# Kernel tuning notes

Measured on AMD Instinct MI355X. Metric: run time of the kernel, lower is better.

The kernel has to match this reference:

```python
import jax, jax.numpy as jnp
import numpy as np

N_POINTS = 2_000_000
IN_CH = 10
UNITS = 32  # out_channels // 2 since last_layer=False
NUM_PILLARS = 30_000
BN_EPS = 1e-3


def setup_inputs() -> dict:
    key = jax.random.key(0)
    k1, k2, k3, k4, k5 = jax.random.split(key, 5)
    inputs = jax.random.normal(k1, (N_POINTS, IN_CH), dtype=jnp.float32)
    unq_inv = jax.random.randint(k2, (N_POINTS,), 0, NUM_PILLARS, dtype=jnp.int32)
    # learned params (nn.Linear bias=False, BatchNorm1d affine, PReLU per-channel, alpha scalar)
    W = jax.random.normal(k3, (UNITS, IN_CH), dtype=jnp.float32) / np.sqrt(IN_CH)
    gamma = jnp.ones((UNITS,), dtype=jnp.float32)
    beta = jnp.zeros((UNITS,), dtype=jnp.float32)
    prelu_a = jnp.full((UNITS,), 0.25, dtype=jnp.float32)  # PReLU default init
    alpha = jnp.array(0.0, dtype=jnp.float32)
    return {"inputs": inputs, "W": W, "gamma": gamma, "beta": beta,
            "prelu_a": prelu_a, "alpha": alpha, "unq_inv": unq_inv,
            "num_pillars": NUM_PILLARS}


def reference(inputs, W, gamma, beta, prelu_a, alpha, unq_inv, num_pillars):
    # Linear (no bias): [N, in] @ [in, units]
    x = jnp.einsum('ni,ui->nu', inputs, W)
    # BatchNorm1d, training-mode forward: batch stats, biased variance
    mean = jnp.mean(x, axis=0)
    var = jnp.var(x, axis=0)
    x = (x - mean) * jax.lax.rsqrt(var + BN_EPS) * gamma + beta
    # PReLU with per-channel slope
    x = jnp.where(x > 0, x, prelu_a * x)
    # segment reductions over pillars
    counts = jax.ops.segment_sum(jnp.ones((x.shape[0], 1), x.dtype), unq_inv,
                                 num_segments=num_pillars)
    feat_max = jax.ops.segment_max(x, unq_inv, num_segments=num_pillars)
    feat_max = jnp.where(counts > 0, feat_max, 0.0)  # empty pillars -> 0 (torch_scatter default)
    feat_sum = jax.ops.segment_sum(x, unq_inv, num_segments=num_pillars)
    feat_mean = feat_sum / jnp.maximum(counts, 1.0)
    a = jax.nn.sigmoid(alpha)
    feat_hybrid = a * feat_max + (1.0 - a) * feat_mean
    # gather back and concat (last_vfe == False)
    return jnp.concatenate([x, feat_hybrid[unq_inv]], axis=1)
```

## Files before the change

### kernel.cpp

```cpp
#include <hip/hip_runtime.h>
#include <math.h>

#define BLOCK 256
#define UNITS 32
#define IN_CH 10
#define STATS_BLOCKS 1024
#define PILLARS 30000
#define BN_EPS 1e-3f
#define SCAN_THREADS 1024
#define SCAN_CHUNK 30

__global__ void __launch_bounds__(BLOCK) stats_kernel(const float* __restrict__ inp,
        const float* __restrict__ W, const int* __restrict__ unq,
        float* __restrict__ partials, int* __restrict__ cnt, int N) {
    __shared__ float Wl[UNITS * IN_CH];
    for (int i = threadIdx.x; i < UNITS * IN_CH; i += BLOCK) Wl[i] = W[i];
    __syncthreads();
    float acc[2 * UNITS];
#pragma unroll
    for (int i = 0; i < 2 * UNITS; i++) acc[i] = 0.f;
    int stride = gridDim.x * BLOCK;
    for (int row = blockIdx.x * BLOCK + threadIdx.x; row < N; row += stride) {
        float r[IN_CH];
        const float2* p2 = (const float2*)(inp + (size_t)row * IN_CH);
#pragma unroll
        for (int k = 0; k < IN_CH / 2; k++) { float2 v = p2[k]; r[2*k] = v.x; r[2*k+1] = v.y; }
        atomicAdd(&cnt[unq[row]], 1);
#pragma unroll
        for (int u = 0; u < UNITS; u++) {
            float x = 0.f;
#pragma unroll
            for (int k = 0; k < IN_CH; k++) x = fmaf(r[k], Wl[u * IN_CH + k], x);
            acc[u] += x;
            acc[UNITS + u] = fmaf(x, x, acc[UNITS + u]);
        }
    }
    int lane = threadIdx.x & 63, wid = threadIdx.x >> 6;
    __shared__ float wpart[4][2 * UNITS];
#pragma unroll
    for (int k = 0; k < 2 * UNITS; k++) {
        float v = acc[k];
#pragma unroll
        for (int off = 32; off > 0; off >>= 1) v += __shfl_down(v, off, 64);
        if (lane == 0) wpart[wid][k] = v;
    }
    __syncthreads();
    if (threadIdx.x < 2 * UNITS) {
        float v = wpart[0][threadIdx.x] + wpart[1][threadIdx.x] +
                  wpart[2][threadIdx.x] + wpart[3][threadIdx.x];
        partials[blockIdx.x * (2 * UNITS) + threadIdx.x] = v;
    }
}

__global__ void __launch_bounds__(BLOCK) bn_finalize_kernel(const float* __restrict__ partials,
        const float* __restrict__ gamma, const float* __restrict__ beta,
        float* __restrict__ params, int nblocks, float invN) {
    int c = threadIdx.x & 63, q = threadIdx.x >> 6;
    float local = 0.f;
    for (int i = q; i < nblocks; i += 4) local += partials[i * 64 + c];
    __shared__ float s[4][64];
    __shared__ float tot[64];
    s[q][c] = local;
    __syncthreads();
    if (threadIdx.x < 64)
        tot[threadIdx.x] = s[0][threadIdx.x] + s[1][threadIdx.x] + s[2][threadIdx.x] + s[3][threadIdx.x];
    __syncthreads();
    if (threadIdx.x < UNITS) {
        int u = threadIdx.x;
        float mean = tot[u] * invN;
        float var = tot[UNITS + u] * invN - mean * mean;
        float scale = gamma[u] * rsqrtf(var + BN_EPS);
        params[u] = scale;
        params[UNITS + u] = beta[u] - mean * scale;
    }
}

__global__ void __launch_bounds__(SCAN_THREADS) scan_kernel(const int* __restrict__ cnt,
        int* __restrict__ off) {
    __shared__ int sh[SCAN_THREADS];
    int t = threadIdx.x;
    int begin = t * SCAN_CHUNK;
    int end = begin + SCAN_CHUNK;
    if (end > PILLARS) end = PILLARS;
    int s = 0;
    for (int i = begin; i < end && i < PILLARS; i++) s += cnt[i];
    sh[t] = s;
    __syncthreads();
    for (int d = 1; d < SCAN_THREADS; d <<= 1) {
        int v = (t >= d) ? sh[t - d] : 0;
        __syncthreads();
        sh[t] += v;
        __syncthreads();
    }
    int run = sh[t] - s;
    for (int i = begin; i < end && i < PILLARS; i++) {
        int c = cnt[i];
        off[i] = run;
        run += c;
    }
}

__global__ void __launch_bounds__(BLOCK) main_kernel(const float* __restrict__ inp,
        const float* __restrict__ W, const float* __restrict__ params,
        const float* __restrict__ prelu_a, const int* __restrict__ unq,
        const int* __restrict__ off, int* __restrict__ cursor,
        float* __restrict__ out, int N) {
    __shared__ float Wl[UNITS * IN_CH];
    __shared__ float sc[UNITS], bi[UNITS], pa[UNITS];
    for (int i = threadIdx.x; i < UNITS * IN_CH; i += BLOCK) Wl[i] = W[i];
    if (threadIdx.x < UNITS) {
        sc[threadIdx.x] = params[threadIdx.x];
        bi[threadIdx.x] = params[UNITS + threadIdx.x];
        pa[threadIdx.x] = prelu_a[threadIdx.x];
    }
    __syncthreads();
    int row = blockIdx.x * BLOCK + threadIdx.x;
    if (row >= N) return;
    float r[IN_CH];
    const float2* p2 = (const float2*)(inp + (size_t)row * IN_CH);
#pragma unroll
    for (int k = 0; k < IN_CH / 2; k++) { float2 v = p2[k]; r[2*k] = v.x; r[2*k+1] = v.y; }
    float y[UNITS];
#pragma unroll
    for (int u = 0; u < UNITS; u++) {
        float x = 0.f;
#pragma unroll
        for (int k = 0; k < IN_CH; k++) x = fmaf(r[k], Wl[u * IN_CH + k], x);
        x = fmaf(x, sc[u], bi[u]);
        y[u] = x > 0.f ? x : pa[u] * x;
    }
    float4* op = (float4*)(out + (size_t)row * 64);
#pragma unroll
    for (int g = 0; g < 8; g++)
        op[g] = make_float4(y[4*g], y[4*g+1], y[4*g+2], y[4*g+3]);
    int p = unq[row];
    int dest = off[p] + atomicAdd(&cursor[p], 1);
    float4* sp = (float4*)(out + (size_t)dest * 64 + 32);
#pragma unroll
    for (int g = 0; g < 8; g++)
        sp[g] = make_float4(y[4*g], y[4*g+1], y[4*g+2], y[4*g+3]);
}

__global__ void __launch_bounds__(BLOCK) reduce_kernel(const float* __restrict__ out,
        const int* __restrict__ cnt, const int* __restrict__ off,
        const float* __restrict__ alpha, float* __restrict__ hybrid) {
    int wid = threadIdx.x >> 6, lane = threadIdx.x & 63;
    int p = blockIdx.x * 4 + wid;
    if (p >= PILLARS) return;
    int n = cnt[p];
    int base = off[p];
    int u = lane & 31, half = lane >> 5;
    float sum = 0.f, mx = -INFINITY;
    for (int i = half; i < n; i += 2) {
        float v = out[(size_t)(base + i) * 64 + 32 + u];
        sum += v;
        mx = fmaxf(mx, v);
    }
    sum += __shfl_xor(sum, 32, 64);
    mx = fmaxf(mx, __shfl_xor(mx, 32, 64));
    if (half == 0) {
        float a = 1.f / (1.f + expf(-alpha[0]));
        float mean = sum / fmaxf((float)n, 1.f);
        float m = (n > 0) ? mx : 0.f;
        hybrid[(size_t)p * 32 + u] = a * m + (1.f - a) * mean;
    }
}

__global__ void __launch_bounds__(BLOCK) gather_kernel(const float* __restrict__ hybrid,
        const int* __restrict__ unq, float* __restrict__ out, int total) {
    int gid = blockIdx.x * BLOCK + threadIdx.x;
    if (gid >= total) return;
    int row = gid >> 3, g = gid & 7;
    int p = unq[row];
    float4 h = ((const float4*)hybrid)[p * 8 + g];
    ((float4*)out)[(size_t)row * 16 + 8 + g] = h;
}

extern "C" void kernel_launch(void* const* d_in, const int* in_sizes, int n_in,
                              void* d_out, int out_size, void* d_ws, size_t ws_size,
                              hipStream_t stream) {
    const float* inp   = (const float*)d_in[0];
    const float* W     = (const float*)d_in[1];
    const float* gamma = (const float*)d_in[2];
    const float* beta  = (const float*)d_in[3];
    const float* pra   = (const float*)d_in[4];
    const float* alpha = (const float*)d_in[5];
    const int*   unq   = (const int*)d_in[6];
    int N = in_sizes[0] / IN_CH;
    float* out = (float*)d_out;

    char* ws = (char*)d_ws;
    float* partials = (float*)ws;
    float* params   = (float*)(ws + 262144);
    int*   cnt      = (int*)(ws + 262400);
    int*   cursor   = (int*)(ws + 382400);
    int*   off      = (int*)(ws + 502400);
    float* hybrid   = (float*)(ws + 622400);

    hipMemsetAsync(ws + 262400, 0, 240000, stream);

    hipLaunchKernelGGL(stats_kernel, dim3(STATS_BLOCKS), dim3(BLOCK), 0, stream,
                       inp, W, unq, partials, cnt, N);
    hipLaunchKernelGGL(bn_finalize_kernel, dim3(1), dim3(BLOCK), 0, stream,
                       partials, gamma, beta, params, STATS_BLOCKS, 1.f / (float)N);
    hipLaunchKernelGGL(scan_kernel, dim3(1), dim3(SCAN_THREADS), 0, stream,
                       cnt, off);
    hipLaunchKernelGGL(main_kernel, dim3((N + BLOCK - 1) / BLOCK), dim3(BLOCK), 0, stream,
                       inp, W, params, pra, unq, off, cursor, out, N);
    hipLaunchKernelGGL(reduce_kernel, dim3((PILLARS + 3) / 4), dim3(BLOCK), 0, stream,
                       out, cnt, off, alpha, hybrid);
    int gtotal = N * 8;
    hipLaunchKernelGGL(gather_kernel, dim3((gtotal + BLOCK - 1) / BLOCK), dim3(BLOCK), 0, stream,
                       hybrid, unq, out, gtotal);
}
```

Measured before the change: 1.118 ms.

## Scatter row indices instead of features; fuse pillar reduce with hybrid writeback

main_kernel no longer writes a second, pillar-sorted copy of each 32-float feature row. It bumps the pillar's offset atomically and records only the row index, which also removes the separate cursor array. reduce_kernel then reads features indirectly through the index list, computes max and mean, and writes the hybrid value straight into each member row's second half, so the hybrid buffer and gather kernel go away. This trades 128-byte scattered writes plus a full gather pass for 4-byte index writes and indirect reads and writes. The indirect accesses are less coalesced, and off now holds end offsets after main runs. Empty pillars are skipped safely because no row references them.

Result: faster. 1.090 ms (-2.4%).

```diff
diff --git a/kernel.cpp b/kernel.cpp
--- a/kernel.cpp
+++ b/kernel.cpp
@@ -83,7 +83,7 @@
     int end = begin + SCAN_CHUNK;
     if (end > PILLARS) end = PILLARS;
     int s = 0;
-    for (int i = begin; i < end && i < PILLARS; i++) s += cnt[i];
+    for (int i = begin; i < end; i++) s += cnt[i];
     sh[t] = s;
     __syncthreads();
     for (int d = 1; d < SCAN_THREADS; d <<= 1) {
@@ -93,7 +93,7 @@
         __syncthreads();
     }
     int run = sh[t] - s;
-    for (int i = begin; i < end && i < PILLARS; i++) {
+    for (int i = begin; i < end; i++) {
         int c = cnt[i];
         off[i] = run;
         run += c;
@@ -103,7 +103,7 @@
 __global__ void __launch_bounds__(BLOCK) main_kernel(const float* __restrict__ inp,
         const float* __restrict__ W, const float* __restrict__ params,
         const float* __restrict__ prelu_a, const int* __restrict__ unq,
-        const int* __restrict__ off, int* __restrict__ cursor,
+        int* __restrict__ off, int* __restrict__ idx,
         float* __restrict__ out, int N) {
     __shared__ float Wl[UNITS * IN_CH];
     __shared__ float sc[UNITS], bi[UNITS], pa[UNITS];
@@ -134,46 +134,37 @@
     for (int g = 0; g < 8; g++)
         op[g] = make_float4(y[4*g], y[4*g+1], y[4*g+2], y[4*g+3]);
     int p = unq[row];
-    int dest = off[p] + atomicAdd(&cursor[p], 1);
-    float4* sp = (float4*)(out + (size_t)dest * 64 + 32);
-#pragma unroll
-    for (int g = 0; g < 8; g++)
-        sp[g] = make_float4(y[4*g], y[4*g+1], y[4*g+2], y[4*g+3]);
-}
-
-__global__ void __launch_bounds__(BLOCK) reduce_kernel(const float* __restrict__ out,
-        const int* __restrict__ cnt, const int* __restrict__ off,
-        const float* __restrict__ alpha, float* __restrict__ hybrid) {
+    int dest = atomicAdd(&off[p], 1);
+    idx[dest] = row;
+}
+
+__global__ void __launch_bounds__(BLOCK) reduce_kernel(float* __restrict__ out,
+        const int* __restrict__ off, const int* __restrict__ idx,
+        const float* __restrict__ alpha) {
     int wid = threadIdx.x >> 6, lane = threadIdx.x & 63;
     int p = blockIdx.x * 4 + wid;
     if (p >= PILLARS) return;
-    int n = cnt[p];
-    int base = off[p];
+    int base = (p == 0) ? 0 : off[p - 1];
+    int end = off[p];
+    if (end <= base) return;
+    int n = end - base;
     int u = lane & 31, half = lane >> 5;
     float sum = 0.f, mx = -INFINITY;
-    for (int i = half; i < n; i += 2) {
-        float v = out[(size_t)(base + i) * 64 + 32 + u];
+    for (int i = base + half; i < end; i += 2) {
+        int row = idx[i];
+        float v = out[(size_t)row * 64 + u];
         sum += v;
         mx = fmaxf(mx, v);
     }
     sum += __shfl_xor(sum, 32, 64);
     mx = fmaxf(mx, __shfl_xor(mx, 32, 64));
-    if (half == 0) {
-        float a = 1.f / (1.f + expf(-alpha[0]));
-        float mean = sum / fmaxf((float)n, 1.f);
-        float m = (n > 0) ? mx : 0.f;
-        hybrid[(size_t)p * 32 + u] = a * m + (1.f - a) * mean;
-    }
-}
-
-__global__ void __launch_bounds__(BLOCK) gather_kernel(const float* __restrict__ hybrid,
-        const int* __restrict__ unq, float* __restrict__ out, int total) {
-    int gid = blockIdx.x * BLOCK + threadIdx.x;
-    if (gid >= total) return;
-    int row = gid >> 3, g = gid & 7;
-    int p = unq[row];
-    float4 h = ((const float4*)hybrid)[p * 8 + g];
-    ((float4*)out)[(size_t)row * 16 + 8 + g] = h;
+    float a = 1.f / (1.f + expf(-alpha[0]));
+    float mean = sum / (float)n;
+    float h = a * mx + (1.f - a) * mean;
+    for (int i = base + half; i < end; i += 2) {
+        int row = idx[i];
+        out[(size_t)row * 64 + 32 + u] = h;
+    }
 }
 
 extern "C" void kernel_launch(void* const* d_in, const int* in_sizes, int n_in,
@@ -190,14 +181,13 @@
     float* out = (float*)d_out;
 
     char* ws = (char*)d_ws;
-    float* partials = (float*)ws;
-    float* params   = (float*)(ws + 262144);
-    int*   cnt      = (int*)(ws + 262400);
-    int*   cursor   = (int*)(ws + 382400);
-    int*   off      = (int*)(ws + 502400);
-    float* hybrid   = (float*)(ws + 622400);
-
-    hipMemsetAsync(ws + 262400, 0, 240000, stream);
+    float* params   = (float*)ws;
+    int*   off      = (int*)(ws + 256);
+    int*   cnt      = (int*)(ws + 120256);
+    float* partials = (float*)(ws + 240256);
+    int*   idx      = (int*)(ws + 502400);
+
+    hipMemsetAsync(cnt, 0, PILLARS * sizeof(int), stream);
 
     hipLaunchKernelGGL(stats_kernel, dim3(STATS_BLOCKS), dim3(BLOCK), 0, stream,
                        inp, W, unq, partials, cnt, N);
@@ -206,10 +196,7 @@
     hipLaunchKernelGGL(scan_kernel, dim3(1), dim3(SCAN_THREADS), 0, stream,
                        cnt, off);
     hipLaunchKernelGGL(main_kernel, dim3((N + BLOCK - 1) / BLOCK), dim3(BLOCK), 0, stream,
-                       inp, W, params, pra, unq, off, cursor, out, N);
+                       inp, W, params, pra, unq, off, idx, out, N);
     hipLaunchKernelGGL(reduce_kernel, dim3((PILLARS + 3) / 4), dim3(BLOCK), 0, stream,
-                       out, cnt, off, alpha, hybrid);
-    int gtotal = N * 8;
-    hipLaunchKernelGGL(gather_kernel, dim3((gtotal + BLOCK - 1) / BLOCK), dim3(BLOCK), 0, stream,
-                       hybrid, unq, out, gtotal);
-}
+                       out, off, idx, alpha);
+}
```
